# Optimization experiments

Hardware: AMD Instinct MI355X
Metric: run time of the kernel (lower is better)

The kernel has to match this reference:

```python
import jax, jax.numpy as jnp
import numpy as np
import math

D_MODEL = 1024
N_HEAD = 16
D_FF = 4096
B, T, S = 2, 2048, 2048
LN_EPS = 1e-5


def _linear(x, w, b):
    # torch nn.Linear: y = x @ W.T + b, W: [out, in]
    return jnp.einsum('bsd,od->bso', x, w) + b


def _layer_norm(x, g, b):
    mu = jnp.mean(x, axis=-1, keepdims=True)
    var = jnp.var(x, axis=-1, keepdims=True)
    return (x - mu) * jax.lax.rsqrt(var + LN_EPS) * g + b


def _mha(xq, xkv, wq, bq, wk, bk, wv, bv, wo, bo, mask):
    Bq, Tq, D = xq.shape
    Tk = xkv.shape[1]
    dk = D // N_HEAD
    q = _linear(xq, wq, bq).reshape(Bq, Tq, N_HEAD, dk).transpose(0, 2, 1, 3)
    k = _linear(xkv, wk, bk).reshape(Bq, Tk, N_HEAD, dk).transpose(0, 2, 1, 3)
    v = _linear(xkv, wv, bv).reshape(Bq, Tk, N_HEAD, dk).transpose(0, 2, 1, 3)
    scores = jnp.einsum('bhqd,bhkd->bhqk', q, k) / math.sqrt(dk)
    if mask is not None:
        scores = jnp.where(mask == 0, jnp.asarray(-1e9, scores.dtype), scores)
    attn = jax.nn.softmax(scores, axis=-1)  # dropout is eval-mode identity
    out = jnp.einsum('bhqk,bhkd->bhqd', attn, v)
    out = out.transpose(0, 2, 1, 3).reshape(Bq, Tq, D)
    return _linear(out, wo, bo)


def setup_inputs() -> dict:
    key = jax.random.key(0)
    ks = jax.random.split(key, 20)
    sd = 0.02

    def w(k, shape):
        return (jax.random.normal(k, shape, dtype=jnp.float32) * sd)

    inp = {
        'x': jax.random.normal(ks[0], (B, T, D_MODEL), dtype=jnp.float32),
        'enc_output': jax.random.normal(ks[1], (B, S, D_MODEL), dtype=jnp.float32),
        # causal (future) mask for self-attention
        'tgt_mask': jnp.tril(jnp.ones((T, T), dtype=jnp.int32))[None, None, :, :].repeat(B, axis=0),
        # no source padding -> all ones
        'src_tgt_mask': jnp.ones((B, 1, T, S), dtype=jnp.int32),
        'sa_wq': w(ks[2], (D_MODEL, D_MODEL)), 'sa_bq': jnp.zeros((D_MODEL,), jnp.float32),
        'sa_wk': w(ks[3], (D_MODEL, D_MODEL)), 'sa_bk': jnp.zeros((D_MODEL,), jnp.float32),
        'sa_wv': w(ks[4], (D_MODEL, D_MODEL)), 'sa_bv': jnp.zeros((D_MODEL,), jnp.float32),
        'sa_wo': w(ks[5], (D_MODEL, D_MODEL)), 'sa_bo': jnp.zeros((D_MODEL,), jnp.float32),
        'ca_wq': w(ks[6], (D_MODEL, D_MODEL)), 'ca_bq': jnp.zeros((D_MODEL,), jnp.float32),
        'ca_wk': w(ks[7], (D_MODEL, D_MODEL)), 'ca_bk': jnp.zeros((D_MODEL,), jnp.float32),
        'ca_wv': w(ks[8], (D_MODEL, D_MODEL)), 'ca_bv': jnp.zeros((D_MODEL,), jnp.float32),
        'ca_wo': w(ks[9], (D_MODEL, D_MODEL)), 'ca_bo': jnp.zeros((D_MODEL,), jnp.float32),
        'ffn_w1': w(ks[10], (D_FF, D_MODEL)), 'ffn_b1': jnp.zeros((D_FF,), jnp.float32),
        'ffn_w2': w(ks[11], (D_MODEL, D_FF)), 'ffn_b2': jnp.zeros((D_MODEL,), jnp.float32),
        'ln1_g': jnp.ones((D_MODEL,), jnp.float32), 'ln1_b': jnp.zeros((D_MODEL,), jnp.float32),
        'ln2_g': jnp.ones((D_MODEL,), jnp.float32), 'ln2_b': jnp.zeros((D_MODEL,), jnp.float32),
        'ln3_g': jnp.ones((D_MODEL,), jnp.float32), 'ln3_b': jnp.zeros((D_MODEL,), jnp.float32),
    }
    return inp


def reference(x, enc_output, tgt_mask, src_tgt_mask,
              sa_wq, sa_bq, sa_wk, sa_bk, sa_wv, sa_bv, sa_wo, sa_bo,
              ca_wq, ca_bq, ca_wk, ca_bk, ca_wv, ca_bv, ca_wo, ca_bo,
              ffn_w1, ffn_b1, ffn_w2, ffn_b2,
              ln1_g, ln1_b, ln2_g, ln2_b, ln3_g, ln3_b):
    # masked self-attention + residual + LN
    a1 = _mha(x, x, sa_wq, sa_bq, sa_wk, sa_bk, sa_wv, sa_bv, sa_wo, sa_bo, tgt_mask)
    x = _layer_norm(x + a1, ln1_g, ln1_b)
    # cross-attention + residual + LN
    a2 = _mha(x, enc_output, ca_wq, ca_bq, ca_wk, ca_bk, ca_wv, ca_bv, ca_wo, ca_bo, src_tgt_mask)
    x = _layer_norm(x + a2, ln2_g, ln2_b)
    # FFN + residual + LN
    h = jax.nn.relu(_linear(x, ffn_w1, ffn_b1))
    f = _linear(h, ffn_w2, ffn_b2)
    x = _layer_norm(x + f, ln3_g, ln3_b)
    return x
```

## Files before the change

### kernel.cpp

```cpp
#include <hip/hip_runtime.h>
#include <stdint.h>

typedef uint16_t u16;
typedef __attribute__((ext_vector_type(8))) short short8;
typedef __attribute__((ext_vector_type(4))) short short4v;
typedef __attribute__((ext_vector_type(4))) float f32x4;
typedef __attribute__((ext_vector_type(2))) unsigned int u32x2;

#define GLB_AS __attribute__((address_space(1)))
#define LDS_AS __attribute__((address_space(3)))

__device__ __forceinline__ void gload_lds16(const void* g, void* l) {
  __builtin_amdgcn_global_load_lds((GLB_AS void*)(g), (LDS_AS void*)(l), 16, 0, 0);
}

__device__ __forceinline__ float bf2f(u16 u) {
  union { uint32_t i; float f; } v; v.i = ((uint32_t)u) << 16; return v.f;
}
__device__ __forceinline__ u16 f2bf(float f) {
  uint32_t x = __builtin_bit_cast(uint32_t, f);
  return (u16)((x + 0x7fffu + ((x >> 16) & 1u)) >> 16);
}
__device__ __forceinline__ uint32_t cvtpk(float lo, float hi) {
  uint32_t r;
  asm("v_cvt_pk_bf16_f32 %0, %1, %2" : "=v"(r) : "v"(lo), "v"(hi));
  return r;
}

struct CastJobs {
  const float* s[12];
  u16* d[12];
  int n[12];
};
__global__ __launch_bounds__(256) void cast_many(CastJobs j)
{
  const int job = blockIdx.y;
  const int i = (blockIdx.x * 256 + threadIdx.x) * 4;
  if (i >= j.n[job]) return;
  const float4 v = *(const float4*)(j.s[job] + i);
  short4v r;
  r[0] = (short)f2bf(v.x); r[1] = (short)f2bf(v.y);
  r[2] = (short)f2bf(v.z); r[3] = (short)f2bf(v.w);
  *(short4v*)(j.d[job] + i) = r;
}

template<int RELU, int NSEG, int BN, int SCALEQ, int VT>
__global__ __launch_bounds__(256) void gemm_bt(
    const u16* __restrict__ A, const u16* __restrict__ W,
    const float* __restrict__ b0, const float* __restrict__ b1,
    const float* __restrict__ b2, u16* __restrict__ Y,
    u16* __restrict__ VTp,
    int M, int N, int K)
{
  __shared__ __attribute__((aligned(16))) u16 lA[2][128*64];
  __shared__ __attribute__((aligned(16))) u16 lB[2][BN*64];
  const int tid  = threadIdx.x;
  const int lane = tid & 63, wv = tid >> 6;
  constexpr int WM = (BN == 128) ? 64 : 32;
  constexpr int MI = WM / 16;
  constexpr int BRND = BN / 32;
  const int wm = (BN == 128) ? (wv >> 1) : wv;
  const int wn = (BN == 128) ? (wv & 1) : 0;
  const int l16 = lane & 15, l4 = lane >> 4;
  const int rswz = (l16 & 7) << 4;

  const int gx = gridDim.x;
  int flat = blockIdx.y * gx + blockIdx.x;
  flat = (flat & 7) * ((gx * gridDim.y) >> 3) + (flat >> 3);
  const int bx = (flat % gx) * BN, by = (flat / gx) * 128;

  const f32x4 fzero = {0.f, 0.f, 0.f, 0.f};
  f32x4 acc[MI][4];
#pragma unroll
  for (int i = 0; i < MI; ++i)
#pragma unroll
    for (int j = 0; j < 4; ++j) acc[i][j] = fzero;

  const int o = wv*1024 + lane*16;

  auto stage = [&](int k0, int buf) {
#pragma unroll
    for (int r = 0; r < 4; ++r) {
      const int oo = r*4096 + o;
      const int row = oo >> 7;
      const int src = ((oo & 127) ^ ((row & 7) << 4)) >> 1;
      gload_lds16(A + (size_t)(by + row)*K + (k0 + src), (char*)lA[buf] + oo);
    }
#pragma unroll
    for (int r = 0; r < BRND; ++r) {
      const int oo = r*4096 + o;
      const int row = oo >> 7;
      const int src = ((oo & 127) ^ ((row & 7) << 4)) >> 1;
      gload_lds16(W + (size_t)(bx + row)*K + (k0 + src), (char*)lB[buf] + oo);
    }
  };

  stage(0, 0);
  const int KT = K >> 6;
  for (int kt = 0; kt < KT; ++kt) {
    const int cur = kt & 1;
    __syncthreads();
    short8 af[2][MI], bfv[2][4];
#pragma unroll
    for (int ks = 0; ks < 2; ++ks) {
      const int cb = (ks*64 + l4*16) ^ rswz;
#pragma unroll
      for (int i = 0; i < MI; ++i)
        af[ks][i]  = *(const short8*)((const char*)lA[cur] + (wm*WM + i*16 + l16)*128 + cb);
#pragma unroll
      for (int j = 0; j < 4; ++j)
        bfv[ks][j] = *(const short8*)((const char*)lB[cur] + (wn*64 + j*16 + l16)*128 + cb);
    }
    if (kt + 1 < KT) stage((kt + 1) << 6, cur ^ 1);
#pragma unroll
    for (int ks = 0; ks < 2; ++ks)
#pragma unroll
      for (int i = 0; i < MI; ++i)
#pragma unroll
        for (int j = 0; j < 4; ++j)
          acc[i][j] = __builtin_amdgcn_mfma_f32_16x16x32_bf16(af[ks][i], bfv[ks][j], acc[i][j], 0, 0, 0);
  }

  const float SCLF = 0.18033688f;
#pragma unroll
  for (int j = 0; j < 4; ++j) {
    const int col = bx + wn*64 + j*16 + l16;
    float bv;
    int seg = 0;
    if (NSEG == 1) bv = b0[col];
    else {
      seg = col >> 10;
      const int off = col & 1023;
      const float* bp = (seg == 0) ? b0 : ((seg == 1) ? b1 : b2);
      bv = bp[off];
    }
#pragma unroll
    for (int i = 0; i < MI; ++i) {
      const int r0 = by + wm*WM + i*16 + l4*4;
      if (VT > 0 && seg == VT) {
        const int dcol = col - (VT << 10);
        const int bb = r0 >> 11, t0 = r0 & 2047;
        short4v pv;
#pragma unroll
        for (int r = 0; r < 4; ++r) pv[r] = (short)f2bf(acc[i][j][r] + bv);
        *(short4v*)(VTp + ((size_t)((bb*16 + (dcol >> 6))*64 + (dcol & 63)))*2048 + t0) = pv;
      } else {
#pragma unroll
        for (int r = 0; r < 4; ++r) {
          float v = acc[i][j][r] + bv;
          if (RELU) v = v > 0.f ? v : 0.f;
          if (SCALEQ && (NSEG == 1 || seg == 0)) v *= SCLF;
          Y[(size_t)(r0 + r)*N + col] = f2bf(v);
        }
      }
    }
  }
}

template<int CAUSAL, int QR>
__global__ __launch_bounds__(512, (QR == 16) ? 4 : 2) void attn_fwd(
    const u16* __restrict__ Q, int qs,
    const u16* __restrict__ K, int ks_,
    const u16* __restrict__ Vt, u16* __restrict__ O, int Tk)
{
  constexpr int NG = QR / 16;
  __shared__ __attribute__((aligned(16))) u16 lK[2][128*64];
  __shared__ __attribute__((aligned(16))) u16 lV[2][64*128];
  __shared__ __attribute__((aligned(16))) u16 lP[8][NG*1024];
  const int tid  = threadIdx.x;
  const int lane = tid & 63, wv = tid >> 6;
  const int l16 = lane & 15, l4 = lane >> 4;
  const int b = blockIdx.z, h = blockIdx.y;
  int strip;
  if (CAUSAL) {
    const int u = (blockIdx.x + blockIdx.z) & 15;
    strip = (u & 1) ? (15 - (u >> 1)) : (u >> 1);
  } else {
    strip = blockIdx.x;
  }
  const int Bq = strip * (8 * QR);
  const int qrow = Bq + wv*QR;

  short8 qf[NG][2];
#pragma unroll
  for (int g = 0; g < NG; ++g) {
    const u16* Qb = Q + (size_t)(b*2048 + qrow + g*16 + l16)*qs + h*64;
#pragma unroll
    for (int ks = 0; ks < 2; ++ks)
      qf[g][ks] = *(const short8*)(Qb + ks*32 + l4*8);
  }

  const f32x4 fzero = {0.f, 0.f, 0.f, 0.f};
  f32x4 accO[NG][4];
#pragma unroll
  for (int g = 0; g < NG; ++g)
#pragma unroll
    for (int i = 0; i < 4; ++i) accO[g][i] = fzero;
  float lrow[NG];
#pragma unroll
  for (int g = 0; g < NG; ++g) lrow[g] = 0.f;

  const int kend = CAUSAL ? (Bq + 8*QR) : Tk;
  const int nt = kend >> 7;
  const int qmax = qrow + QR - 1;
  const int srK = tid >> 3;
  const int scK = 8 * ((tid & 7) ^ (srK & 7));
  const int srV = tid >> 4;
  const int scV = 8 * ((tid & 15) ^ (srV & 7));
  const u16* KbG = K  + (size_t)(b*2048)*ks_ + h*64 + scK;
  const u16* VbG = Vt + ((size_t)((b*16 + h)*64 + srV))*2048 + scV;
  const int wvoff = (tid >> 6) * 1024;
  const int rswz = (l16 & 7) << 4;
  const int sbq = (lane & 48) + l4*4;

  char* const pbuf = (char*)lP + (tid >> 6) * (NG*2048);
  const int swzP = (l16 & 7) << 4;
  int wrA[4], rdA[2];
#pragma unroll
  for (int nf = 0; nf < 4; ++nf) wrA[nf] = l16*128 + ((nf*32 + l4*8) ^ swzP);
#pragma unroll
  for (int c = 0; c < 2; ++c)    rdA[c] = l16*128 + ((c*64 + l4*16) ^ swzP);

  auto readK = [&](int h2, int bb, short8 (&kf)[4][2]) {
#pragma unroll
    for (int nf = 0; nf < 4; ++nf) {
      const char* base = (const char*)lK[bb] + (h2*64 + nf*16 + l16)*128;
      kf[nf][0] = *(const short8*)(base + ((l4*16)      ^ rswz));
      kf[nf][1] = *(const short8*)(base + ((64 + l4*16) ^ rswz));
    }
  };

  auto compute64 = [&](int h2, int kvb, short8 (&kf)[4][2], int bb) {
#pragma unroll
    for (int g = 0; g < NG; ++g) {
      f32x4 sf[4];
      __builtin_amdgcn_s_setprio(1);
#pragma unroll
      for (int nf = 0; nf < 4; ++nf) {
        f32x4 s = fzero;
        s = __builtin_amdgcn_mfma_f32_16x16x32_bf16(kf[nf][0], qf[g][0], s, 0, 0, 0);
        s = __builtin_amdgcn_mfma_f32_16x16x32_bf16(kf[nf][1], qf[g][1], s, 0, 0, 0);
        sf[nf] = s;
      }
      __builtin_amdgcn_s_setprio(0);
      if (CAUSAL && (kvb + 63 > qrow + g*16)) {
        const int q = qrow + g*16 + l16;
#pragma unroll
        for (int nf = 0; nf < 4; ++nf)
#pragma unroll
          for (int r = 0; r < 4; ++r) {
            const int kv = kvb + nf*16 + l4*4 + r;
            if (kv > q) sf[nf][r] = -1e30f;
          }
      }
#pragma unroll
      for (int nf = 0; nf < 4; ++nf)
#pragma unroll
        for (int r = 0; r < 4; ++r)
          sf[nf][r] = exp2f(sf[nf][r]);
      float sm[4];
#pragma unroll
      for (int nf = 0; nf < 4; ++nf)
        sm[nf] = (sf[nf][0] + sf[nf][1]) + (sf[nf][2] + sf[nf][3]);
      lrow[g] += (sm[0] + sm[1]) + (sm[2] + sm[3]);
#pragma unroll
      for (int nf = 0; nf < 4; ++nf) {
        u32x2 w;
        w[0] = cvtpk(sf[nf][0], sf[nf][1]);
        w[1] = cvtpk(sf[nf][2], sf[nf][3]);
        *(u32x2*)(pbuf + g*2048 + wrA[nf]) = w;
      }
    }
#pragma unroll
    for (int c = 0; c < 2; ++c) {
      short8 pa[NG];
#pragma unroll
      for (int g = 0; g < NG; ++g)
        pa[g] = *(const short8*)(pbuf + g*2048 + rdA[c]);
      __builtin_amdgcn_s_setprio(1);
#pragma unroll
      for (int df = 0; df < 4; ++df) {
        const short8 vf = *(const short8*)((const char*)lV[bb] +
            (df*16 + l16)*256 + ((h2*128 + c*64 + l4*16) ^ rswz));
#pragma unroll
        for (int g = 0; g < NG; ++g)
          accO[g][df] = __builtin_amdgcn_mfma_f32_16x16x32_bf16(pa[g], vf, accO[g][df], 0, 0, 0);
      }
      __builtin_amdgcn_s_setprio(0);
    }
  };

#pragma unroll
  for (int r = 0; r < 2; ++r) {
    gload_lds16(KbG + (size_t)(r*64 + srK)*ks_, (char*)lK[0] + r*8192 + wvoff);
    gload_lds16(VbG + (size_t)(r*32)*2048,      (char*)lV[0] + r*8192 + wvoff);
  }

  for (int t = 0; t < nt; ++t) {
    const int bb = t & 1;
    const int kb = t << 7;
    __syncthreads();
    short8 kf[4][2];
    readK(0, bb, kf);
    if (t + 1 < nt) {
      const int kb2 = kb + 128;
#pragma unroll
      for (int r = 0; r < 2; ++r) {
        gload_lds16(KbG + (size_t)(kb2 + r*64 + srK)*ks_,
                    (char*)lK[bb^1] + r*8192 + wvoff);
        gload_lds16(VbG + (size_t)(r*32)*2048 + kb2,
                    (char*)lV[bb^1] + r*8192 + wvoff);
      }
    }
    compute64(0, kb, kf, bb);
    if (!CAUSAL || (kb + 64 <= qmax)) {
      readK(1, bb, kf);
      compute64(1, kb + 64, kf, bb);
    }
  }

#pragma unroll
  for (int g = 0; g < NG; ++g) {
    lrow[g] += __shfl_xor(lrow[g], 16);
    lrow[g] += __shfl_xor(lrow[g], 32);
    u16* Ob = O + (size_t)(b*2048 + qrow + g*16 + l4*4)*1024 + h*64;
#pragma unroll
    for (int r = 0; r < 4; ++r) {
      const float inv = 1.f / __shfl(lrow[g], sbq + r);
#pragma unroll
      for (int df = 0; df < 4; ++df)
        Ob[(size_t)r*1024 + df*16 + l16] = f2bf(accO[g][df][r] * inv);
    }
  }
}

template<int XF32, int OF32>
__global__ __launch_bounds__(256) void add_ln(
    const void* __restrict__ Xp, const u16* __restrict__ R,
    const float* __restrict__ G, const float* __restrict__ Bb,
    void* __restrict__ OUTp)
{
  const int row  = blockIdx.x*4 + (threadIdx.x >> 6);
  const int lane = threadIdx.x & 63;
  const size_t base = (size_t)row*1024 + lane*16;
  float v[16];
  if (XF32) {
#pragma unroll
    for (int k = 0; k < 4; ++k) {
      const float4 t = *(const float4*)((const float*)Xp + base + k*4);
      v[k*4+0] = t.x; v[k*4+1] = t.y; v[k*4+2] = t.z; v[k*4+3] = t.w;
    }
  } else {
#pragma unroll
    for (int k = 0; k < 2; ++k) {
      short8 t = *(const short8*)((const u16*)Xp + base + k*8);
#pragma unroll
      for (int i = 0; i < 8; ++i) v[k*8+i] = bf2f((u16)t[i]);
    }
  }
#pragma unroll
  for (int k = 0; k < 2; ++k) {
    short8 t = *(const short8*)(R + base + k*8);
#pragma unroll
    for (int i = 0; i < 8; ++i) v[k*8+i] += bf2f((u16)t[i]);
  }
  float s = 0.f, s2 = 0.f;
#pragma unroll
  for (int i = 0; i < 16; ++i) { s += v[i]; s2 += v[i]*v[i]; }
#pragma unroll
  for (int m = 1; m < 64; m <<= 1) { s += __shfl_xor(s, m); s2 += __shfl_xor(s2, m); }
  const float mu  = s * (1.f/1024.f);
  const float var = s2 * (1.f/1024.f) - mu*mu;
  const float rs  = rsqrtf(var + 1e-5f);
  float gg[16], bb_[16];
#pragma unroll
  for (int k = 0; k < 4; ++k) {
    const float4 g4 = *(const float4*)(G  + lane*16 + k*4);
    const float4 b4 = *(const float4*)(Bb + lane*16 + k*4);
    gg[k*4+0]=g4.x; gg[k*4+1]=g4.y; gg[k*4+2]=g4.z; gg[k*4+3]=g4.w;
    bb_[k*4+0]=b4.x; bb_[k*4+1]=b4.y; bb_[k*4+2]=b4.z; bb_[k*4+3]=b4.w;
  }
  if (OF32) {
#pragma unroll
    for (int k = 0; k < 4; ++k) {
      float4 ov;
      ov.x = (v[k*4+0]-mu)*rs*gg[k*4+0] + bb_[k*4+0];
      ov.y = (v[k*4+1]-mu)*rs*gg[k*4+1] + bb_[k*4+1];
      ov.z = (v[k*4+2]-mu)*rs*gg[k*4+2] + bb_[k*4+2];
      ov.w = (v[k*4+3]-mu)*rs*gg[k*4+3] + bb_[k*4+3];
      *(float4*)((float*)OUTp + base + k*4) = ov;
    }
  } else {
#pragma unroll
    for (int k = 0; k < 2; ++k) {
      short8 ov;
#pragma unroll
      for (int i = 0; i < 8; ++i)
        ov[i] = (short)f2bf((v[k*8+i]-mu)*rs*gg[k*8+i] + bb_[k*8+i]);
      *(short8*)((u16*)OUTp + base + k*8) = ov;
    }
  }
}

extern "C" void kernel_launch(void* const* d_in, const int* in_sizes, int n_in,
                              void* d_out, int out_size, void* d_ws, size_t ws_size,
                              hipStream_t stream)
{
  (void)in_sizes; (void)n_in; (void)out_size;
  const float* x    = (const float*)d_in[0];
  const float* enc  = (const float*)d_in[1];
  const float* sa_wq = (const float*)d_in[4];  const float* sa_bq = (const float*)d_in[5];
  const float* sa_wk = (const float*)d_in[6];  const float* sa_bk = (const float*)d_in[7];
  const float* sa_wv = (const float*)d_in[8];  const float* sa_bv = (const float*)d_in[9];
  const float* sa_wo = (const float*)d_in[10]; const float* sa_bo = (const float*)d_in[11];
  const float* ca_wq = (const float*)d_in[12]; const float* ca_bq = (const float*)d_in[13];
  const float* ca_wk = (const float*)d_in[14]; const float* ca_bk = (const float*)d_in[15];
  const float* ca_wv = (const float*)d_in[16]; const float* ca_bv = (const float*)d_in[17];
  const float* ca_wo = (const float*)d_in[18]; const float* ca_bo = (const float*)d_in[19];
  const float* w1 = (const float*)d_in[20];    const float* b1 = (const float*)d_in[21];
  const float* w2 = (const float*)d_in[22];    const float* b2 = (const float*)d_in[23];
  const float* ln1g = (const float*)d_in[24];  const float* ln1b = (const float*)d_in[25];
  const float* ln2g = (const float*)d_in[26];  const float* ln2b = (const float*)d_in[27];
  const float* ln3g = (const float*)d_in[28];  const float* ln3b = (const float*)d_in[29];
  float* out = (float*)d_out;

  char* ws = (char*)d_ws;
  const size_t MB = 1024*1024;
  u16* xb   = (u16*)(ws);
  u16* encb = (u16*)(ws + 8*MB);
  u16* wsab = (u16*)(ws + 16*MB);
  u16* wcab = (u16*)(ws + 24*MB);
  u16* x1   = (u16*)(ws + 32*MB);
  u16* ao   = (u16*)(ws + 40*MB);
  u16* tmp  = (u16*)(ws + 48*MB);
  u16* vt   = (u16*)(ws + 56*MB);
  u16* qkv  = (u16*)(ws + 64*MB);
  u16* kvb  = (u16*)(ws + 88*MB);
  u16* x2   = xb;
  u16* hb   = qkv;

  const bool bigws = ws_size >= (size_t)120*MB;
  u16* w1b = bigws ? (u16*)(ws + 104*MB) : encb;
  u16* w2b = bigws ? (u16*)(ws + 112*MB) : vt;

  const int NW = 1024*1024;
  const int NX = 4096*1024;
  dim3 blk(256);

  {
    CastJobs cj{};
    cj.s[0] = x;     cj.d[0] = xb;           cj.n[0] = NX;
    cj.s[1] = enc;   cj.d[1] = encb;         cj.n[1] = NX;
    cj.s[2] = sa_wq; cj.d[2] = wsab + 0*NW;  cj.n[2] = NW;
    cj.s[3] = sa_wk; cj.d[3] = wsab + 1*NW;  cj.n[3] = NW;
    cj.s[4] = sa_wv; cj.d[4] = wsab + 2*NW;  cj.n[4] = NW;
    cj.s[5] = sa_wo; cj.d[5] = wsab + 3*NW;  cj.n[5] = NW;
    cj.s[6] = ca_wq; cj.d[6] = wcab + 0*NW;  cj.n[6] = NW;
    cj.s[7] = ca_wk; cj.d[7] = wcab + 1*NW;  cj.n[7] = NW;
    cj.s[8] = ca_wv; cj.d[8] = wcab + 2*NW;  cj.n[8] = NW;
    cj.s[9] = ca_wo; cj.d[9] = wcab + 3*NW;  cj.n[9] = NW;
    int njobs = 10;
    if (bigws) {
      cj.s[10] = w1; cj.d[10] = w1b; cj.n[10] = NX;
      cj.s[11] = w2; cj.d[11] = w2b; cj.n[11] = NX;
      njobs = 12;
    }
    cast_many<<<dim3(NX/1024, njobs), blk, 0, stream>>>(cj);
  }

  const int M = 4096;
  dim3 gN64(16, 32);
  dim3 gQKV(24, 32);
  dim3 gKV(16, 32);
  dim3 gF1(32, 32);
  dim3 gAttn(16, 16, 2);
  dim3 blk512(512);

  gemm_bt<0,3,128,1,2><<<gQKV, blk, 0, stream>>>(xb, wsab, sa_bq, sa_bk, sa_bv, qkv, vt, M, 3072, 1024);
  attn_fwd<1,16><<<gAttn, blk512, 0, stream>>>(qkv, 3072, qkv + 1024, 3072, vt, ao, 2048);
  gemm_bt<0,1,64,0,0><<<gN64, blk, 0, stream>>>(ao, wsab + 3*NW, sa_bo, sa_bo, sa_bo, tmp, nullptr, M, 1024, 1024);
  add_ln<1,0><<<1024, blk, 0, stream>>>(x, tmp, ln1g, ln1b, x1);

  gemm_bt<0,1,64,1,0><<<gN64, blk, 0, stream>>>(x1, wcab + 0*NW, ca_bq, ca_bq, ca_bq, qkv, nullptr, M, 1024, 1024);
  gemm_bt<0,2,128,0,1><<<gKV, blk, 0, stream>>>(encb, wcab + 1*NW, ca_bk, ca_bv, ca_bv, kvb, vt, M, 2048, 1024);
  attn_fwd<0,16><<<gAttn, blk512, 0, stream>>>(qkv, 1024, kvb, 2048, vt, ao, 2048);
  if (!bigws) {
    CastJobs cj{};
    cj.s[0] = w1; cj.d[0] = w1b; cj.n[0] = NX;
    cj.s[1] = w2; cj.d[1] = w2b; cj.n[1] = NX;
    cast_many<<<dim3(NX/1024, 2), blk, 0, stream>>>(cj);
  }
  gemm_bt<0,1,64,0,0><<<gN64, blk, 0, stream>>>(ao, wcab + 3*NW, ca_bo, ca_bo, ca_bo, tmp, nullptr, M, 1024, 1024);
  add_ln<0,0><<<1024, blk, 0, stream>>>(x1, tmp, ln2g, ln2b, x2);

  gemm_bt<1,1,128,0,0><<<gF1, blk, 0, stream>>>(x2, w1b, b1, b1, b1, hb, nullptr, M, 4096, 1024);
  gemm_bt<0,1,64,0,0><<<gN64, blk, 0, stream>>>(hb, w2b, b2, b2, b2, tmp, nullptr, M, 1024, 4096);
  add_ln<0,1><<<1024, blk, 0, stream>>>(x2, tmp, ln3g, ln3b, out);
}
```

Baseline: 320.4 us.

## Add 256x256-tile bf16 GEMM kernel for FFN first layer

Introduces a dedicated 512-thread GEMM with 256x256 output tiles, double-buffered direct-to-LDS loads with XOR swizzle, and an 8-way grouped block remap, and uses it for the FFN up-projection with ReLU. Larger tiles raise arithmetic intensity and cut global/LDS traffic per FLOP compared with the previous 128-wide tile kernel. In exchange it uses 128 KB of LDS and many accumulator registers per block, so occupancy drops to one block per CU. The grid shrinks to 256 blocks, which may leave the machine underfilled.

```diff
diff --git a/kernel.cpp b/kernel.cpp
--- a/kernel.cpp
+++ b/kernel.cpp
@@ -152,6 +152,118 @@
           if (SCALEQ && (NSEG == 1 || seg == 0)) v *= SCLF;
           Y[(size_t)(r0 + r)*N + col] = f2bf(v);
         }
+      }
+    }
+  }
+}
+
+template<int RELU>
+__global__ __launch_bounds__(512) void gemm256(
+    const u16* __restrict__ A, const u16* __restrict__ W,
+    const float* __restrict__ b0, u16* __restrict__ Y,
+    int M, int N, int K)
+{
+  __shared__ __attribute__((aligned(16))) u16 lA[2][256*64];
+  __shared__ __attribute__((aligned(16))) u16 lB[2][256*64];
+  const int tid  = threadIdx.x;
+  const int lane = tid & 63, wid = tid >> 6;
+  const int wm = wid >> 2, wn = wid & 3;
+  const int l16 = lane & 15, l4 = lane >> 4;
+  const int rswz = (l16 & 7) << 4;
+
+  const int gx = gridDim.x;
+  int flat = blockIdx.y * gx + blockIdx.x;
+  flat = (flat & 7) * ((gx * gridDim.y) >> 3) + (flat >> 3);
+  const int bx = (flat % gx) * 256, by = (flat / gx) * 256;
+
+  const f32x4 fzero = {0.f, 0.f, 0.f, 0.f};
+  f32x4 acc[8][4];
+#pragma unroll
+  for (int i = 0; i < 8; ++i)
+#pragma unroll
+    for (int j = 0; j < 4; ++j) acc[i][j] = fzero;
+
+  const int o = tid * 16;
+
+  auto stage = [&](int k0, int buf) {
+#pragma unroll
+    for (int r = 0; r < 4; ++r) {
+      const int oo = r*8192 + o;
+      const int row = oo >> 7;
+      const int src = ((oo & 127) ^ ((row & 7) << 4)) >> 1;
+      gload_lds16(A + (size_t)(by + row)*K + (k0 + src), (char*)lA[buf] + oo);
+    }
+#pragma unroll
+    for (int r = 0; r < 4; ++r) {
+      const int oo = r*8192 + o;
+      const int row = oo >> 7;
+      const int src = ((oo & 127) ^ ((row & 7) << 4)) >> 1;
+      gload_lds16(W + (size_t)(bx + row)*K + (k0 + src), (char*)lB[buf] + oo);
+    }
+  };
+
+  stage(0, 0);
+  const int KT = K >> 6;
+  for (int kt = 0; kt < KT; ++kt) {
+    const int cur = kt & 1;
+    __syncthreads();
+    short8 bfv[2][4];
+#pragma unroll
+    for (int ks = 0; ks < 2; ++ks) {
+      const int cb = (ks*64 + l4*16) ^ rswz;
+#pragma unroll
+      for (int j = 0; j < 4; ++j)
+        bfv[ks][j] = *(const short8*)((const char*)lB[cur] + (wn*64 + j*16 + l16)*128 + cb);
+    }
+    short8 af[2][2];
+#pragma unroll
+    for (int ks = 0; ks < 2; ++ks) {
+      const int cb = (ks*64 + l4*16) ^ rswz;
+#pragma unroll
+      for (int i = 0; i < 2; ++i)
+        af[ks][i] = *(const short8*)((const char*)lA[cur] + (wm*128 + i*16 + l16)*128 + cb);
+    }
+    if (kt + 1 < KT) stage((kt + 1) << 6, cur ^ 1);
+#pragma unroll
+    for (int ks = 0; ks < 2; ++ks)
+#pragma unroll
+      for (int i = 0; i < 2; ++i)
+#pragma unroll
+        for (int j = 0; j < 4; ++j)
+          acc[i][j] = __builtin_amdgcn_mfma_f32_16x16x32_bf16(af[ks][i], bfv[ks][j], acc[i][j], 0, 0, 0);
+#pragma unroll
+    for (int q = 1; q < 4; ++q) {
+#pragma unroll
+      for (int ks = 0; ks < 2; ++ks) {
+        const int cb = (ks*64 + l4*16) ^ rswz;
+#pragma unroll
+        for (int i = 0; i < 2; ++i)
+          af[ks][i] = *(const short8*)((const char*)lA[cur] +
+              (wm*128 + (q*2 + i)*16 + l16)*128 + cb);
+      }
+#pragma unroll
+      for (int ks = 0; ks < 2; ++ks)
+#pragma unroll
+        for (int i = 0; i < 2; ++i)
+#pragma unroll
+          for (int j = 0; j < 4; ++j)
+            acc[q*2 + i][j] = __builtin_amdgcn_mfma_f32_16x16x32_bf16(
+                af[ks][i], bfv[ks][j], acc[q*2 + i][j], 0, 0, 0);
+    }
+  }
+
+#pragma unroll
+  for (int j = 0; j < 4; ++j) {
+    const int col = bx + wn*64 + j*16 + l16;
+    const float bv = b0[col];
+#pragma unroll
+    for (int i = 0; i < 8; ++i) {
+      const int r0 = by + wm*128 + i*16 + l4*4;
+#pragma unroll
+      for (int r = 0; r < 4; ++r) {
+        float v = acc[i][j][r] + bv;
+        if (RELU) v = v > 0.f ? v : 0.f;
+        Y[(size_t)(r0 + r)*N + col] = f2bf(v);
       }
     }
   }
@@ -472,7 +584,7 @@
   dim3 gN64(16, 32);
   dim3 gQKV(24, 32);
   dim3 gKV(16, 32);
-  dim3 gF1(32, 32);
+  dim3 gF1(16, 16);
   dim3 gAttn(16, 16, 2);
   dim3 blk512(512);
 
@@ -493,7 +605,7 @@
   gemm_bt<0,1,64,0,0><<<gN64, blk, 0, stream>>>(ao, wcab + 3*NW, ca_bo, ca_bo, ca_bo, tmp, nullptr, M, 1024, 1024);
   add_ln<0,0><<<1024, blk, 0, stream>>>(x1, tmp, ln2g, ln2b, x2);
 
-  gemm_bt<1,1,128,0,0><<<gF1, blk, 0, stream>>>(x2, w1b, b1, b1, b1, hb, nullptr, M, 4096, 1024);
+  gemm256<1><<<gF1, blk512, 0, stream>>>(x2, w1b, b1, hb, M, 4096, 1024);
   gemm_bt<0,1,64,0,0><<<gN64, blk, 0, stream>>>(hb, w2b, b2, b2, b2, tmp, nullptr, M, 1024, 4096);
   add_ln<0,1><<<1024, blk, 0, stream>>>(x2, tmp, ln3g, ln3b, out);
 }
```

New measurement: 323.5 us. Within noise of the previous version (+1.0%).
